# Optimization experiments

Measured on AMD Instinct MI355X. Metric: run time of the kernel, lower is better.

Reference implementation:

```python
import jax, jax.numpy as jnp
import numpy as np

Z, Y, X = 200, 8, 200
XM, YM, ZM = 80.0, 6.0, 80.0  # x_meter, y_meter, z_meter
IMG_H, IMG_W = 256, 512
FEAT_C, OUT_CH = 64, 128
EPS = 1e-8


def create_grid3d():
    # matches torch create_grid3d flattening order (z, y, x), x/y shifted by -0.5
    zz, yy, xx = jnp.meshgrid(jnp.linspace(0.0, 1.0, Z),
                              jnp.linspace(0.0, 1.0, Y),
                              jnp.linspace(0.0, 1.0, X), indexing='ij')
    xyz = jnp.stack([xx.ravel() - 0.5, yy.ravel() - 0.5, zz.ravel()], axis=1)  # (N,3)
    return xyz * jnp.array([XM, YM, ZM], dtype=jnp.float32)


def setup_inputs() -> dict:
    key = jax.random.key(0)
    k1, k2, k3 = jax.random.split(key, 3)
    B = 2
    img_feat = jax.random.normal(k1, (B, FEAT_C, 32, 64), dtype=jnp.float32)
    # realistic pinhole intrinsics so many voxels project in-bounds
    K = jnp.array([[300.0, 0.0, IMG_W / 2.0],
                   [0.0, 300.0, IMG_H / 2.0],
                   [0.0, 0.0, 1.0]], dtype=jnp.float32)
    pix_T_cam = jnp.tile(K[None], (B, 1, 1))
    conv_w = jax.random.normal(k2, (OUT_CH, FEAT_C * Y), dtype=jnp.float32) * 0.02
    conv_b = jax.random.normal(k3, (OUT_CH,), dtype=jnp.float32) * 0.02
    return {"img_feat": img_feat, "pix_T_cam": pix_T_cam, "conv_w": conv_w, "conv_b": conv_b}


def reference(img_feat, pix_T_cam, conv_w, conv_b):
    B, C, H, W = img_feat.shape
    xyz = create_grid3d()  # (N,3), N = Z*Y*X
    pix = jnp.einsum('bij,nj->bni', pix_T_cam, xyz)  # (B,N,3)
    d = pix[..., 2]
    u01 = pix[..., 0] / (d + EPS) / IMG_W  # normalized [0,1] u
    v01 = pix[..., 1] / (d + EPS) / IMG_H
    valid = (u01 >= 0) & (v01 >= 0) & (u01 <= 1) & (v01 <= 1)  # (B,N)

    # grid_sample, align_corners=False, padding_mode='zeros' (D=1 collapses to bilinear)
    gx = u01 * 2.0 - 1.0
    gy = v01 * 2.0 - 1.0
    xp = ((gx + 1.0) * W - 1.0) * 0.5
    yp = ((gy + 1.0) * H - 1.0) * 0.5
    x0f = jnp.floor(xp); y0f = jnp.floor(yp)
    wx1 = xp - x0f; wy1 = yp - y0f
    x0 = x0f.astype(jnp.int32); y0 = y0f.astype(jnp.int32)
    bidx = jnp.arange(B)[:, None]

    def gather(xi, yi):
        ok = (xi >= 0) & (xi < W) & (yi >= 0) & (yi < H)
        xc = jnp.clip(xi, 0, W - 1)
        yc = jnp.clip(yi, 0, H - 1)
        vals = img_feat[bidx, :, yc, xc]  # (B,N,C)
        return vals * ok[..., None].astype(img_feat.dtype)

    v00 = gather(x0, y0)
    v01_ = gather(x0 + 1, y0)
    v10 = gather(x0, y0 + 1)
    v11 = gather(x0 + 1, y0 + 1)
    samp = (v00 * ((1 - wx1) * (1 - wy1))[..., None]
            + v01_ * (wx1 * (1 - wy1))[..., None]
            + v10 * ((1 - wx1) * wy1)[..., None]
            + v11 * (wx1 * wy1)[..., None])  # (B,N,C)
    samp = samp * valid[..., None].astype(samp.dtype)

    bev = samp.reshape(B, Z, Y, X, C)
    # rearrange 'b c d h w -> b (c h) d w' with d=Z, h=Y, w=X
    bev = jnp.transpose(bev, (0, 4, 2, 1, 3)).reshape(B, C * Y, Z, X)
    out = jnp.einsum('bczx,oc->bozx', bev, conv_w) + conv_b[None, :, None, None]
    return out
```

## Files before the change

### kernel.cpp

```cpp
#include <hip/hip_runtime.h>


#define NPOS 40000

typedef short bf16x8 __attribute__((ext_vector_type(8)));
typedef float f32x4  __attribute__((ext_vector_type(4)));

__device__ __forceinline__ unsigned rne16(float f) {
    unsigned u = __float_as_uint(f);
    return (u + 0x7fffu + ((u >> 16) & 1u)) >> 16;
}
__device__ __forceinline__ float lo16(unsigned u) { return __uint_as_float(u << 16); }
__device__ __forceinline__ float hi16(unsigned u) { return __uint_as_float(u & 0xffff0000u); }
__device__ __forceinline__ unsigned cvtpk(float lo, float hi) {
    unsigned r;
    asm("v_cvt_pk_bf16_f32 %0, %1, %2" : "=v"(r) : "v"(lo), "v"(hi));
    return r;
}

__global__ __launch_bounds__(256)
void bili_prep(const float* __restrict__ img, const float* __restrict__ convw,
               unsigned short* __restrict__ imgT, unsigned short* __restrict__ Wp)
{
    const int i = blockIdx.x * 256 + threadIdx.x;
    if (blockIdx.x < 1024) {
        const int c = i & 63, x = (i >> 6) & 63, y = (i >> 12) & 31, b = i >> 17;
        imgT[i] = (unsigned short)rne16(img[((b * 64 + c) * 32 + y) * 64 + x]);
    } else {
        const int j = i - 1024 * 256;
        const int k = j & 511, o = j >> 9;
        const int y = k >> 6, c = k & 63;
        Wp[j] = (unsigned short)rne16(convw[o * 512 + c * 8 + y]);
    }
}

__global__ __launch_bounds__(256, 3)
void bili_main(const uint4* __restrict__ imgTq,
               const unsigned short* __restrict__ Wp,
               const float* __restrict__ pixT,
               const float* __restrict__ convb,
               float* __restrict__ out)
{
    __shared__ uint4  Fb[2][1024];
    __shared__ uint2  offsC[512];
    __shared__ float4 wtsL[512];

    const int t   = threadIdx.x;
    const int bx  = blockIdx.x;
    const int b   = (bx >= 625) ? 1 : 0;
    const int n0  = (bx - b * 625) * 64;

    const int wv  = t >> 6;
    const int ln  = t & 63;
    const int l15 = ln & 15;
    const int lg  = ln >> 4;
    const int g   = t >> 3;
    const int li  = t & 7;

    f32x4 acc0[4], acc1[4];
    {
        float bias0[4], bias1[4];
        #pragma unroll
        for (int r = 0; r < 4; ++r) {
            bias0[r] = convb[wv * 32 +      lg * 4 + r];
            bias1[r] = convb[wv * 32 + 16 + lg * 4 + r];
        }
        #pragma unroll
        for (int nt = 0; nt < 4; ++nt)
            #pragma unroll
            for (int r = 0; r < 4; ++r) { acc0[nt][r] = bias0[r]; acc1[nt][r] = bias1[r]; }
    }

    {
        const float* Kb = pixT + b * 9;
        const float K00 = Kb[0], K01 = Kb[1], K02 = Kb[2];
        const float K10 = Kb[3], K11 = Kb[4], K12 = Kb[5];
        const float K20 = Kb[6], K21 = Kb[7], K22 = Kb[8];

        #pragma unroll
        for (int r = 0; r < 2; ++r) {
            const int p    = r * 256 + t;
            const int nloc = p >> 3;
            const int y    = p & 7;
            const int n = n0 + nloc;
            const int z = n / 200;
            const int x = n - z * 200;

            const float pxv = (x * (1.0f / 199.0f) - 0.5f) * 80.0f;
            const float pzv = (z * (1.0f / 199.0f)) * 80.0f;
            const float pyv = (y * (1.0f / 7.0f) - 0.5f) * 6.0f;

            const float p0 = K00 * pxv + K01 * pyv + K02 * pzv;
            const float p1 = K10 * pxv + K11 * pyv + K12 * pzv;
            const float d  = K20 * pxv + K21 * pyv + K22 * pzv;
            const float inv = __builtin_amdgcn_rcpf(d + 1e-8f);
            const float u01 = p0 * inv * (1.0f / 512.0f);
            const float v01 = p1 * inv * (1.0f / 256.0f);
            const float vf = (u01 >= 0.0f && u01 <= 1.0f &&
                              v01 >= 0.0f && v01 <= 1.0f) ? 1.0f : 0.0f;

            float xp = u01 * 64.0f - 0.5f;
            xp = fminf(fmaxf(xp, -2.0f), 66.0f);
            const float x0f = floorf(xp);
            const float wx = xp - x0f;
            const int x0 = (int)x0f, x1i = x0 + 1;
            const float wx0 = (1.0f - wx) * vf * ((x0  >= 0 && x0  < 64) ? 1.0f : 0.0f);
            const float wx1 = wx          * vf * ((x1i >= 0 && x1i < 64) ? 1.0f : 0.0f);
            const int xi0 = min(max(x0, 0), 63);
            const int xi1 = min(max(x1i, 0), 63);

            float yp = v01 * 32.0f - 0.5f;
            yp = fminf(fmaxf(yp, -2.0f), 34.0f);
            const float y0f = floorf(yp);
            const float wy = yp - y0f;
            const int y0 = (int)y0f, y1i = y0 + 1;
            const float wy0 = (1.0f - wy) * ((y0  >= 0 && y0  < 32) ? 1.0f : 0.0f);
            const float wy1 = wy          * ((y1i >= 0 && y1i < 32) ? 1.0f : 0.0f);
            const int yi0 = min(max(y0, 0), 31);
            const int yi1 = min(max(y1i, 0), 31);

            const unsigned o0 = (unsigned)(((yi0 << 6) + xi0) << 3);
            const unsigned o1 = (unsigned)(((yi0 << 6) + xi1) << 3);
            const unsigned o2 = (unsigned)(((yi1 << 6) + xi0) << 3);
            const unsigned o3 = (unsigned)(((yi1 << 6) + xi1) << 3);

            wtsL[p]  = make_float4(wx0 * wy0, wx1 * wy0, wx0 * wy1, wx1 * wy1);
            offsC[p] = make_uint2(o0 | (o1 << 16), o2 | (o3 << 16));
        }
    }

    __syncthreads();

    const uint4*  imgTb = imgTq + b * 16384;
    const bf16x8* ApG   = (const bf16x8*)Wp;
    const bf16x8* Ap0   = ApG + ((wv * 32 +      l15) * 64 + lg);
    const bf16x8* Ap1   = ApG + ((wv * 32 + 16 + l15) * 64 + lg);

    uint4 sbE[8], sbO[8];

    #define ISSUE_H(q, hb, SB)                                                 \
        _Pragma("unroll")                                                      \
        for (int it2 = 0; it2 < 2; ++it2) {                                    \
            const int pp = ((hb) * 2 + it2) * 32 + g;                          \
            const int n_ = pp >> 1, ys = pp & 1;                               \
            const int p_ = n_ * 8 + 2 * (q) + ys;                              \
            const uint2 oc = offsC[p_];                                        \
            SB[it2 * 4 + 0] = imgTb[(oc.x & 0xffffu) + li];                    \
            SB[it2 * 4 + 1] = imgTb[(oc.x >> 16)     + li];                    \
            SB[it2 * 4 + 2] = imgTb[(oc.y & 0xffffu) + li];                    \
            SB[it2 * 4 + 3] = imgTb[(oc.y >> 16)     + li];                    \
        }

    #define PROC_H(q, hb, SB, buf)                                             \
        _Pragma("unroll")                                                      \
        for (int it2 = 0; it2 < 2; ++it2) {                                    \
            const int pp = ((hb) * 2 + it2) * 32 + g;                          \
            const int n_ = pp >> 1, ys = pp & 1;                               \
            const int p_ = n_ * 8 + 2 * (q) + ys;                              \
            const float4 w = wtsL[p_];                                         \
            float2 ac[4];                                                      \
            _Pragma("unroll")                                                  \
            for (int qq = 0; qq < 4; ++qq) ac[qq] = make_float2(0.0f, 0.0f);   \
            _Pragma("unroll")                                                  \
            for (int j = 0; j < 4; ++j) {                                      \
                const uint4 v = SB[it2 * 4 + j];                               \
                const float ww = (j == 0) ? w.x : (j == 1) ? w.y : (j == 2) ? w.z : w.w; \
                ac[0].x = fmaf(ww, lo16(v.x), ac[0].x);                        \
                ac[0].y = fmaf(ww, hi16(v.x), ac[0].y);                        \
                ac[1].x = fmaf(ww, lo16(v.y), ac[1].x);                        \
                ac[1].y = fmaf(ww, hi16(v.y), ac[1].y);                        \
                ac[2].x = fmaf(ww, lo16(v.z), ac[2].x);                        \
                ac[2].y = fmaf(ww, hi16(v.z), ac[2].y);                        \
                ac[3].x = fmaf(ww, lo16(v.w), ac[3].x);                        \
                ac[3].y = fmaf(ww, hi16(v.w), ac[3].y);                        \
            }                                                                  \
            uint4 pk;                                                          \
            pk.x = cvtpk(ac[0].x, ac[0].y);                                    \
            pk.y = cvtpk(ac[1].x, ac[1].y);                                    \
            pk.z = cvtpk(ac[2].x, ac[2].y);                                    \
            pk.w = cvtpk(ac[3].x, ac[3].y);                                    \
            (buf)[n_ * 16 + ((ys * 8 + li) ^ (n_ & 7))] = pk;                  \
        }

    #define MFMA_H(q, hf, buf)                                                 \
        do {                                                                   \
            const bf16x8* Fv = (const bf16x8*)(buf);                           \
            _Pragma("unroll")                                                  \
            for (int k2 = 0; k2 < 2; ++k2) {                                   \
                const int k = (hf) * 2 + k2;                                   \
                const bf16x8 a0_ = Ap0[((q) * 4 + k) * 4];                     \
                const bf16x8 a1_ = Ap1[((q) * 4 + k) * 4];                     \
                _Pragma("unroll")                                              \
                for (int nt = 0; nt < 4; ++nt) {                               \
                    const int nn = nt * 16 + l15;                              \
                    const bf16x8 bv = Fv[nn * 16 + ((k * 4 + lg) ^ (nn & 7))]; \
                    acc0[nt] = __builtin_amdgcn_mfma_f32_16x16x32_bf16(a0_, bv, acc0[nt], 0, 0, 0); \
                    acc1[nt] = __builtin_amdgcn_mfma_f32_16x16x32_bf16(a1_, bv, acc1[nt], 0, 0, 0); \
                }                                                              \
            }                                                                  \
        } while (0)

    ISSUE_H(0, 0, sbE);
    ISSUE_H(0, 1, sbO);
    PROC_H (0, 0, sbE, Fb[0]);
    ISSUE_H(1, 0, sbE);
    PROC_H (0, 1, sbO, Fb[0]);
    __syncthreads();

    ISSUE_H(1, 1, sbO);
    MFMA_H (0, 0, Fb[0]);
    PROC_H (1, 0, sbE, Fb[1]);
    ISSUE_H(2, 0, sbE);
    MFMA_H (0, 1, Fb[0]);
    PROC_H (1, 1, sbO, Fb[1]);
    __syncthreads();

    ISSUE_H(2, 1, sbO);
    MFMA_H (1, 0, Fb[1]);
    PROC_H (2, 0, sbE, Fb[0]);
    ISSUE_H(3, 0, sbE);
    MFMA_H (1, 1, Fb[1]);
    PROC_H (2, 1, sbO, Fb[0]);
    __syncthreads();

    ISSUE_H(3, 1, sbO);
    MFMA_H (2, 0, Fb[0]);
    PROC_H (3, 0, sbE, Fb[1]);
    MFMA_H (2, 1, Fb[0]);
    PROC_H (3, 1, sbO, Fb[1]);
    __syncthreads();

    MFMA_H (3, 0, Fb[1]);
    MFMA_H (3, 1, Fb[1]);

    #undef ISSUE_H
    #undef PROC_H
    #undef MFMA_H

    {
        float* ob = out + (size_t)(b * 128 + wv * 32) * NPOS + n0;
        #pragma unroll
        for (int nt = 0; nt < 4; ++nt) {
            #pragma unroll
            for (int r = 0; r < 4; ++r) {
                ob[(     lg * 4 + r) * NPOS + nt * 16 + l15] = acc0[nt][r];
                ob[(16 + lg * 4 + r) * NPOS + nt * 16 + l15] = acc1[nt][r];
            }
        }
    }
}

extern "C" void kernel_launch(void* const* d_in, const int* in_sizes, int n_in,
                              void* d_out, int out_size, void* d_ws, size_t ws_size,
                              hipStream_t stream) {
    const float* img   = (const float*)d_in[0];
    const float* pixT  = (const float*)d_in[1];
    const float* convw = (const float*)d_in[2];
    const float* convb = (const float*)d_in[3];
    float* out = (float*)d_out;

    unsigned short* imgT = (unsigned short*)d_ws;
    unsigned short* Wp   = imgT + 262144;

    hipLaunchKernelGGL(bili_prep, dim3(1280), dim3(256), 0, stream,
                       img, convw, imgT, Wp);
    hipLaunchKernelGGL(bili_main, dim3(1250), dim3(256), 0, stream,
                       (const uint4*)imgT, Wp, pixT, convb, out);
}
```

Before: 43.56 us.

## Vectorize prep packing, use byte offsets, packed FMA, setprio and lighter barriers

```diff
diff --git a/kernel.cpp b/kernel.cpp
--- a/kernel.cpp
+++ b/kernel.cpp
@@ -17,17 +17,34 @@
     asm("v_cvt_pk_bf16_f32 %0, %1, %2" : "=v"(r) : "v"(lo), "v"(hi));
     return r;
 }
+__device__ __forceinline__ void pkfma(float2& a, float2 v, float2 w) {
+    asm("v_pk_fma_f32 %0, %1, %2, %0" : "+v"(a) : "v"(v), "v"(w));
+}
+__device__ __forceinline__ void tile_barrier() {
+    asm volatile("s_waitcnt lgkmcnt(0)" ::: "memory");
+    __builtin_amdgcn_s_barrier();
+    __builtin_amdgcn_sched_barrier(0);
+}
 
 __global__ __launch_bounds__(256)
 void bili_prep(const float* __restrict__ img, const float* __restrict__ convw,
                unsigned short* __restrict__ imgT, unsigned short* __restrict__ Wp)
 {
-    const int i = blockIdx.x * 256 + threadIdx.x;
-    if (blockIdx.x < 1024) {
-        const int c = i & 63, x = (i >> 6) & 63, y = (i >> 12) & 31, b = i >> 17;
-        imgT[i] = (unsigned short)rne16(img[((b * 64 + c) * 32 + y) * 64 + x]);
+    const int t = threadIdx.x;
+    if (blockIdx.x < 128) {
+        const int u   = blockIdx.x * 256 + t;
+        const int li8 = u & 7, x = (u >> 3) & 63, y = (u >> 9) & 31, b = u >> 14;
+        const float* src = img + (((b * 64 + li8 * 8) * 32 + y) * 64 + x);
+        unsigned pk[4];
+        #pragma unroll
+        for (int cc = 0; cc < 8; ++cc) {
+            const unsigned v = rne16(src[cc * 2048]);
+            if ((cc & 1) == 0) pk[cc >> 1] = v;
+            else               pk[cc >> 1] |= (v << 16);
+        }
+        ((uint4*)imgT)[u] = make_uint4(pk[0], pk[1], pk[2], pk[3]);
     } else {
-        const int j = i - 1024 * 256;
+        const int j = (blockIdx.x - 128) * 256 + t;
         const int k = j & 511, o = j >> 9;
         const int y = k >> 6, c = k & 63;
         Wp[j] = (unsigned short)rne16(convw[o * 512 + c * 8 + y]);
@@ -35,14 +52,14 @@
 }
 
 __global__ __launch_bounds__(256, 3)
-void bili_main(const uint4* __restrict__ imgTq,
+void bili_main(const char* __restrict__ imgTbytes,
                const unsigned short* __restrict__ Wp,
                const float* __restrict__ pixT,
                const float* __restrict__ convb,
                float* __restrict__ out)
 {
     __shared__ uint4  Fb[2][1024];
-    __shared__ uint2  offsC[512];
+    __shared__ uint4  offsB[512];
     __shared__ float4 wtsL[512];
 
     const int t   = threadIdx.x;
@@ -55,7 +72,7 @@
     const int l15 = ln & 15;
     const int lg  = ln >> 4;
     const int g   = t >> 3;
-    const int li  = t & 7;
+    const unsigned liOff = (unsigned)((t & 7) << 4);
 
     f32x4 acc0[4], acc1[4];
     {
@@ -119,19 +136,19 @@
             const int yi0 = min(max(y0, 0), 31);
             const int yi1 = min(max(y1i, 0), 31);
 
-            const unsigned o0 = (unsigned)(((yi0 << 6) + xi0) << 3);
-            const unsigned o1 = (unsigned)(((yi0 << 6) + xi1) << 3);
-            const unsigned o2 = (unsigned)(((yi1 << 6) + xi0) << 3);
-            const unsigned o3 = (unsigned)(((yi1 << 6) + xi1) << 3);
+            const unsigned o0 = (unsigned)(((yi0 << 6) + xi0) << 7);
+            const unsigned o1 = (unsigned)(((yi0 << 6) + xi1) << 7);
+            const unsigned o2 = (unsigned)(((yi1 << 6) + xi0) << 7);
+            const unsigned o3 = (unsigned)(((yi1 << 6) + xi1) << 7);
 
             wtsL[p]  = make_float4(wx0 * wy0, wx1 * wy0, wx0 * wy1, wx1 * wy1);
-            offsC[p] = make_uint2(o0 | (o1 << 16), o2 | (o3 << 16));
-        }
-    }
-
-    __syncthreads();
-
-    const uint4*  imgTb = imgTq + b * 16384;
+            offsB[p] = make_uint4(o0, o1, o2, o3);
+        }
+    }
+
+    tile_barrier();
+
+    const char*   imgTb = imgTbytes + (size_t)b * 262144;
     const bf16x8* ApG   = (const bf16x8*)Wp;
     const bf16x8* Ap0   = ApG + ((wv * 32 +      l15) * 64 + lg);
     const bf16x8* Ap1   = ApG + ((wv * 32 + 16 + l15) * 64 + lg);
@@ -144,11 +161,11 @@
             const int pp = ((hb) * 2 + it2) * 32 + g;                          \
             const int n_ = pp >> 1, ys = pp & 1;                               \
             const int p_ = n_ * 8 + 2 * (q) + ys;                              \
-            const uint2 oc = offsC[p_];                                        \
-            SB[it2 * 4 + 0] = imgTb[(oc.x & 0xffffu) + li];                    \
-            SB[it2 * 4 + 1] = imgTb[(oc.x >> 16)     + li];                    \
-            SB[it2 * 4 + 2] = imgTb[(oc.y & 0xffffu) + li];                    \
-            SB[it2 * 4 + 3] = imgTb[(oc.y >> 16)     + li];                    \
+            const uint4 oc = offsB[p_];                                        \
+            SB[it2 * 4 + 0] = *(const uint4*)(imgTb + (size_t)(oc.x | liOff)); \
+            SB[it2 * 4 + 1] = *(const uint4*)(imgTb + (size_t)(oc.y | liOff)); \
+            SB[it2 * 4 + 2] = *(const uint4*)(imgTb + (size_t)(oc.z | liOff)); \
+            SB[it2 * 4 + 3] = *(const uint4*)(imgTb + (size_t)(oc.w | liOff)); \
         }
 
     #define PROC_H(q, hb, SB, buf)                                             \
@@ -165,26 +182,29 @@
             for (int j = 0; j < 4; ++j) {                                      \
                 const uint4 v = SB[it2 * 4 + j];                               \
                 const float ww = (j == 0) ? w.x : (j == 1) ? w.y : (j == 2) ? w.z : w.w; \
-                ac[0].x = fmaf(ww, lo16(v.x), ac[0].x);                        \
-                ac[0].y = fmaf(ww, hi16(v.x), ac[0].y);                        \
-                ac[1].x = fmaf(ww, lo16(v.y), ac[1].x);                        \
-                ac[1].y = fmaf(ww, hi16(v.y), ac[1].y);                        \
-                ac[2].x = fmaf(ww, lo16(v.z), ac[2].x);                        \
-                ac[2].y = fmaf(ww, hi16(v.z), ac[2].y);                        \
-                ac[3].x = fmaf(ww, lo16(v.w), ac[3].x);                        \
-                ac[3].y = fmaf(ww, hi16(v.w), ac[3].y);                        \
+                const float2 w2 = make_float2(ww, ww);                         \
+                float2 t0, t1, t2, t3;                                         \
+                t0.x = lo16(v.x); t0.y = hi16(v.x);                            \
+                t1.x = lo16(v.y); t1.y = hi16(v.y);                            \
+                t2.x = lo16(v.z); t2.y = hi16(v.z);                            \
+                t3.x = lo16(v.w); t3.y = hi16(v.w);                            \
+                pkfma(ac[0], t0, w2);                                          \
+                pkfma(ac[1], t1, w2);                                          \
+                pkfma(ac[2], t2, w2);                                          \
+                pkfma(ac[3], t3, w2);                                          \
             }                                                                  \
             uint4 pk;                                                          \
             pk.x = cvtpk(ac[0].x, ac[0].y);                                    \
             pk.y = cvtpk(ac[1].x, ac[1].y);                                    \
             pk.z = cvtpk(ac[2].x, ac[2].y);                                    \
             pk.w = cvtpk(ac[3].x, ac[3].y);                                    \
-            (buf)[n_ * 16 + ((ys * 8 + li) ^ (n_ & 7))] = pk;                  \
+            (buf)[n_ * 16 + ((ys * 8 + (t & 7)) ^ (n_ & 7))] = pk;             \
         }
 
     #define MFMA_H(q, hf, buf)                                                 \
         do {                                                                   \
             const bf16x8* Fv = (const bf16x8*)(buf);                           \
+            __builtin_amdgcn_s_setprio(1);                                     \
             _Pragma("unroll")                                                  \
             for (int k2 = 0; k2 < 2; ++k2) {                                   \
                 const int k = (hf) * 2 + k2;                                   \
@@ -198,6 +218,7 @@
                     acc1[nt] = __builtin_amdgcn_mfma_f32_16x16x32_bf16(a1_, bv, acc1[nt], 0, 0, 0); \
                 }                                                              \
             }                                                                  \
+            __builtin_amdgcn_s_setprio(0);                                     \
         } while (0)
 
     ISSUE_H(0, 0, sbE);
@@ -205,7 +226,7 @@
     PROC_H (0, 0, sbE, Fb[0]);
     ISSUE_H(1, 0, sbE);
     PROC_H (0, 1, sbO, Fb[0]);
-    __syncthreads();
+    tile_barrier();
 
     ISSUE_H(1, 1, sbO);
     MFMA_H (0, 0, Fb[0]);
@@ -213,7 +234,7 @@
     ISSUE_H(2, 0, sbE);
     MFMA_H (0, 1, Fb[0]);
     PROC_H (1, 1, sbO, Fb[1]);
-    __syncthreads();
+    tile_barrier();
 
     ISSUE_H(2, 1, sbO);
     MFMA_H (1, 0, Fb[1]);
@@ -221,14 +242,14 @@
     ISSUE_H(3, 0, sbE);
     MFMA_H (1, 1, Fb[1]);
     PROC_H (2, 1, sbO, Fb[0]);
-    __syncthreads();
+    tile_barrier();
 
     ISSUE_H(3, 1, sbO);
     MFMA_H (2, 0, Fb[0]);
     PROC_H (3, 0, sbE, Fb[1]);
     MFMA_H (2, 1, Fb[0]);
     PROC_H (3, 1, sbO, Fb[1]);
-    __syncthreads();
+    tile_barrier();
 
     MFMA_H (3, 0, Fb[1]);
     MFMA_H (3, 1, Fb[1]);
@@ -262,8 +283,8 @@
     unsigned short* imgT = (unsigned short*)d_ws;
     unsigned short* Wp   = imgT + 262144;
 
-    hipLaunchKernelGGL(bili_prep, dim3(1280), dim3(256), 0, stream,
+    hipLaunchKernelGGL(bili_prep, dim3(384), dim3(256), 0, stream,
                        img, convw, imgT, Wp);
     hipLaunchKernelGGL(bili_main, dim3(1250), dim3(256), 0, stream,
-                       (const uint4*)imgT, Wp, pixT, convb, out);
-}
+                       (const char*)imgT, Wp, pixT, convb, out);
+}
```

Result: slower. 48.44 us (+11.2%).
